# Optimization experiments

Hardware: AMD Instinct MI355X
Metric: run time of the kernel (lower is better)

## Reference

```python
import jax, jax.numpy as jnp
import numpy as np

B, S, D, H = 2, 2048, 512, 8
E = D // H  # per-head depth = 64


def setup_inputs() -> dict:
    key = jax.random.key(0)
    ks = jax.random.split(key, 10)
    x = jax.random.normal(ks[0], (B, S, D), dtype=jnp.float32)
    # binary mask: 1 = masked position (added as -1e9)
    attention_mask = jax.random.randint(ks[1], (B, S, S), 0, 2, dtype=jnp.int32)
    # per-head Dense weights stacked: [H, D, E] (Keras Dense: y = x @ W + b)
    sc = 1.0 / np.sqrt(D)
    Wq = jax.random.normal(ks[2], (H, D, E), dtype=jnp.float32) * sc
    Wk = jax.random.normal(ks[3], (H, D, E), dtype=jnp.float32) * sc
    Wv = jax.random.normal(ks[4], (H, D, E), dtype=jnp.float32) * sc
    bq = jnp.zeros((H, E), dtype=jnp.float32)
    bk = jnp.zeros((H, E), dtype=jnp.float32)
    bv = jnp.zeros((H, E), dtype=jnp.float32)
    Wo = jax.random.normal(ks[5], (D, D), dtype=jnp.float32) * sc
    bo = jnp.zeros((D,), dtype=jnp.float32)
    return {"x": x, "attention_mask": attention_mask, "Wq": Wq, "bq": bq,
            "Wk": Wk, "bk": bk, "Wv": Wv, "bv": bv, "Wo": Wo, "bo": bo}


def reference(x, attention_mask, Wq, bq, Wk, bk, Wv, bv, Wo, bo):
    # Per-head Dense projections, vectorized over heads: [B,H,S,E]
    q = jnp.einsum('bsd,hde->bhse', x, Wq) + bq[None, :, None, :]
    k = jnp.einsum('bsd,hde->bhse', x, Wk) + bk[None, :, None, :]
    v = jnp.einsum('bsd,hde->bhse', x, Wv) + bv[None, :, None, :]
    # scaled dot-product attention
    scores = jnp.einsum('bhse,bhte->bhst', q, k) / jnp.sqrt(jnp.float32(E))
    scores = scores + (-1e9) * attention_mask.astype(jnp.float32)[:, None, :, :]
    weights = jax.nn.softmax(scores, axis=-1)
    o = jnp.einsum('bhst,bhte->bhse', weights, v)
    # concat heads (head i -> columns [i*E:(i+1)*E]) then output Dense
    o = o.transpose(0, 2, 1, 3).reshape(B, S, D)
    return o @ Wo + bo
```

## Files before the change

### kernel.cpp

```cpp
#include <hip/hip_runtime.h>
#include <hip/hip_bf16.h>

typedef unsigned short u16;
typedef unsigned int u32;
typedef unsigned long long u64;
typedef short s16x8 __attribute__((ext_vector_type(8)));
typedef float f32x4 __attribute__((ext_vector_type(4)));
typedef float f32x16 __attribute__((ext_vector_type(16)));
typedef int i32x4 __attribute__((ext_vector_type(4)));

static __device__ __forceinline__ u16 f2b(float f) {
    union { float f; unsigned u; } x; x.f = f;
    unsigned r = x.u + 0x7fffu + ((x.u >> 16) & 1u);
    return (u16)(r >> 16);
}

static __device__ __forceinline__ u32 pkbf2(float a, float b) {
    union { __hip_bfloat162 h; u32 u; } c;
    c.h = __float22bfloat162_rn(make_float2(a, b));
    return c.u;
}

static __device__ __forceinline__ f32x16 zero16() {
    f32x16 z;
#pragma unroll
    for (int i = 0; i < 16; i++) z[i] = 0.f;
    return z;
}

static __device__ __forceinline__ s16x8 mk8(u32 a, u32 b, u32 c, u32 d) {
    union { u32 u[4]; s16x8 v; } x;
    x.u[0] = a; x.u[1] = b; x.u[2] = c; x.u[3] = d;
    return x.v;
}

static __device__ __forceinline__ u32 sx32(u32 v) {
    return (u32)__shfl_xor((int)v, 32, 64);
}

static __device__ __forceinline__ void gll16(const u16* g, u16* l) {
    __builtin_amdgcn_global_load_lds(
        (const __attribute__((address_space(1))) u32*)g,
        (__attribute__((address_space(3))) u32*)l, 16, 0, 0);
}


__global__ __launch_bounds__(256)
void k_pack_all(const float* __restrict__ x,
                const float* __restrict__ Wq, const float* __restrict__ Wk,
                const float* __restrict__ Wv, const float* __restrict__ Wo,
                const float* __restrict__ bq, const float* __restrict__ bk,
                const float* __restrict__ bv, const float* __restrict__ bo,
                u16* __restrict__ xb, u16* __restrict__ WT, u16* __restrict__ WoT,
                float* __restrict__ bias) {
    int idx = blockIdx.x * 256 + threadIdx.x;
    if (idx < 524288) {
        int i = idx * 4;
        float4 v = *(const float4*)(x + i);
        ushort4 o;
        o.x = f2b(v.x); o.y = f2b(v.y); o.z = f2b(v.z); o.w = f2b(v.w);
        *(ushort4*)(xb + i) = o;
    } else if (idx < 1310720) {
        int t = idx - 524288;
        int z = t >> 18, r = t & 262143;
        const float* W = (z == 0) ? Wq : (z == 1) ? Wk : Wv;
        int n = r >> 9, d = r & 511;
        WT[t] = f2b(W[((n >> 6) * 512 + d) * 64 + (n & 63)]);
    } else if (idx < 1572864) {
        int r = idx - 1310720;
        int n = r >> 9, d = r & 511;
        WoT[r] = f2b(Wo[d * 512 + n]);
    } else if (idx < 1574912) {
        int i = idx - 1572864;
        float v;
        if (i < 512) v = bq[i];
        else if (i < 1024) v = bk[i - 512];
        else if (i < 1536) v = bv[i - 1024];
        else v = bo[i - 1536];
        bias[i] = v;
    }
}


template<int MF, bool F32OUT>
__global__ __launch_bounds__(256)
void k_gemm(const u16* __restrict__ A, const u16* __restrict__ BTbase,
            const float* __restrict__ biasBase,
            u16* __restrict__ Cb, u16* __restrict__ Vt, float* __restrict__ Cf,
            const int* __restrict__ mask, u32* __restrict__ mb) {
    const int BM = MF * 32;
    const int nblk = blockIdx.x, mblk = blockIdx.y, z = blockIdx.z;
    const int tid = threadIdx.x;

    if (!F32OUT && z == 3) {
        const int bi = mblk * 4 + nblk;
#pragma unroll
        for (int it = 0; it < 4; it++) {
            const int i2 = bi * 1024 + it * 256 + tid;
            const int* p = mask + (size_t)i2 * 32;
            unsigned wv2 = 0;
#pragma unroll
            for (int j = 0; j < 32; j += 4) {
                int4 v = *(const int4*)(p + j);
                wv2 |= ((unsigned)(v.x & 1) << j) | ((unsigned)(v.y & 1) << (j + 1)) |
                       ((unsigned)(v.z & 1) << (j + 2)) | ((unsigned)(v.w & 1) << (j + 3));
            }
            mb[i2] = wv2;
        }
        return;
    }

    const u16* BT = BTbase + (size_t)z * 262144;
    const float* bias = biasBase + z * 512;
    __shared__ __align__(16) u16 As[MF * 32 * 64];
    __shared__ __align__(16) u16 Bs[128 * 64];
    const int lane = tid & 63, wv = tid >> 6;
    const int lr = lane & 15, lg = lane >> 4;
    const int wr = (wv >> 1) * (MF * 16), wc = (wv & 1) * 64;
    const int lr8 = lane >> 3, lc8 = (lane & 7) ^ lr8;
    const u16* Ag = A + (size_t)(mblk * BM + wv * 8 + lr8) * 512 + lc8 * 8;
    const u16* Bg = BT + (size_t)(nblk * 128 + wv * 8 + lr8) * 512 + lc8 * 8;

    f32x4 acc[MF][4];
#pragma unroll
    for (int i = 0; i < MF; i++)
#pragma unroll
        for (int j = 0; j < 4; j++) acc[i][j] = (f32x4){0.f, 0.f, 0.f, 0.f};

    for (int kt = 0; kt < 8; kt++) {
        __syncthreads();
#pragma unroll
        for (int i = 0; i < MF; i++)
            gll16(Ag + (size_t)(i * 32) * 512 + kt * 64, &As[(i * 32 + wv * 8) * 64]);
#pragma unroll
        for (int i = 0; i < 4; i++)
            gll16(Bg + (size_t)(i * 32) * 512 + kt * 64, &Bs[(i * 32 + wv * 8) * 64]);
        __syncthreads();
#pragma unroll
        for (int ks = 0; ks < 2; ks++) {
            s16x8 af[MF], bf[4];
#pragma unroll
            for (int mf = 0; mf < MF; mf++) {
                int r = wr + mf * 16 + lr;
                af[mf] = *(const s16x8*)&As[r * 64 + ((ks * 32 + lg * 8) ^ ((r & 7) << 3))];
            }
#pragma unroll
            for (int nf = 0; nf < 4; nf++) {
                int r = wc + nf * 16 + lr;
                bf[nf] = *(const s16x8*)&Bs[r * 64 + ((ks * 32 + lg * 8) ^ ((r & 7) << 3))];
            }
#pragma unroll
            for (int mf = 0; mf < MF; mf++)
#pragma unroll
                for (int nf = 0; nf < 4; nf++)
                    acc[mf][nf] = __builtin_amdgcn_mfma_f32_16x16x32_bf16(
                        af[mf], bf[nf], acc[mf][nf], 0, 0, 0);
        }
    }
    const float qsc = (!F32OUT && z == 0) ? 0.18033688011112042f : 1.0f;
#pragma unroll
    for (int nf = 0; nf < 4; nf++) {
        int col = nblk * 128 + wc + nf * 16 + lr;
        float bval = bias[col];
#pragma unroll
        for (int mf = 0; mf < MF; mf++) {
            int row0 = mblk * BM + wr + mf * 16 + lg * 4;
            if (F32OUT) {
#pragma unroll
                for (int r = 0; r < 4; r++)
                    Cf[(size_t)(row0 + r) * 512 + col] = acc[mf][nf][r] + bval;
            } else if (z == 2) {
                ushort4 o;
                o.x = f2b(acc[mf][nf][0] + bval);
                o.y = f2b(acc[mf][nf][1] + bval);
                o.z = f2b(acc[mf][nf][2] + bval);
                o.w = f2b(acc[mf][nf][3] + bval);
                *(ushort4*)(Vt + (size_t)(row0 >> 11) * 1048576 +
                            (size_t)col * 2048 + (row0 & 2047)) = o;
            } else {
#pragma unroll
                for (int r = 0; r < 4; r++)
                    Cb[(size_t)z * 2097152 + (size_t)(row0 + r) * 512 + col] =
                        f2b((acc[mf][nf][r] + bval) * qsc);
            }
        }
    }
}


__global__ __launch_bounds__(256, 2)
void k_attn(const u16* __restrict__ qkv, const u16* __restrict__ vt,
            const u32* __restrict__ mb, u16* __restrict__ oc) {
    const int qt = blockIdx.x, h = blockIdx.y, b = blockIdx.z;
    const u16* Qb = qkv + (size_t)b * 1048576 + h * 64;
    const u16* Kb = Qb + 2097152;
    const u16* VtH = vt + (size_t)b * 1048576 + (size_t)h * 131072;

    __shared__ __align__(16) u16 SMEM[24576];
    __shared__ float Lbuf[4][64];

    const int tid = threadIdx.x;
    const int lane = tid & 63, w = tid >> 6;
    const int hi = lane >> 5, l31 = lane & 31;
    const int qrow = qt * 64 + l31;

    const u32* mbl = mb + (size_t)(b * 2048 + qrow) * 64 + w * 16;
    const u32* mbh = mbl + 2048;
    u32 ML[16], MH[16];
#pragma unroll
    for (int i = 0; i < 4; i++) {
        uint4 a = *(const uint4*)(mbl + 4 * i);
        uint4 c = *(const uint4*)(mbh + 4 * i);
        ML[4 * i] = a.x; ML[4 * i + 1] = a.y; ML[4 * i + 2] = a.z; ML[4 * i + 3] = a.w;
        MH[4 * i] = c.x; MH[4 * i + 1] = c.y; MH[4 * i + 2] = c.z; MH[4 * i + 3] = c.w;
    }

    s16x8 qfl[4], qfh[4];
#pragma unroll
    for (int ks = 0; ks < 4; ks++) {
        qfl[ks] = *(const s16x8*)(Qb + (size_t)qrow * 512 + ks * 16 + hi * 8);
        qfh[ks] = *(const s16x8*)(Qb + (size_t)(qrow + 32) * 512 + ks * 16 + hi * 8);
    }

    const int lr8 = lane >> 3, lc8 = (lane & 7) ^ lr8;
    const int vr16 = lane >> 2, vc4 = (lane & 3) ^ ((lane >> 3) & 3);
    const int kv0 = w * 512;

    const u16* kptr = Kb + (size_t)(kv0 + lr8) * 512 + lc8 * 8;
    const u16* vptr = VtH + (size_t)vr16 * 2048 + kv0 + vc4 * 8;

    u16* wbase = &SMEM[w * 6144];
    u16* Vq = wbase + 4096;

    const int kswz = (l31 & 7) << 3;
    const int vkey = (l31 >> 1) & 3;

#pragma unroll
    for (int i = 0; i < 4; i++)
        gll16(kptr + (size_t)(i * 8) * 512, wbase + i * 512);
#pragma unroll
    for (int i = 0; i < 4; i++)
        gll16(vptr + (size_t)(i * 16) * 2048, Vq + i * 512);
#pragma unroll
    for (int i = 0; i < 4; i++)
        gll16(kptr + (size_t)(32 + i * 8) * 512, wbase + 2048 + i * 512);
    asm volatile("s_waitcnt vmcnt(8)" ::: "memory");
    __builtin_amdgcn_sched_barrier(0);

    f32x16 aL0 = zero16(), aL1 = zero16(), aH0 = zero16(), aH1 = zero16();
    f32x4 lvl = (f32x4){0.f, 0.f, 0.f, 0.f}, lvh = (f32x4){0.f, 0.f, 0.f, 0.f};

    f32x16 sl = zero16(), sh = zero16();
    __builtin_amdgcn_s_setprio(1);
#pragma unroll
    for (int ks = 0; ks < 4; ks++) {
        s16x8 kf = *(const s16x8*)&wbase[l31 * 64 + ((ks * 16 + hi * 8) ^ kswz)];
        sl = __builtin_amdgcn_mfma_f32_32x32x16_bf16(kf, qfl[ks], sl, 0, 0, 0);
        sh = __builtin_amdgcn_mfma_f32_32x32x16_bf16(kf, qfh[ks], sh, 0, 0, 0);
    }
    __builtin_amdgcn_s_setprio(0);

#pragma unroll
    for (int t = 0; t < 16; t++) {
        if (t < 14) {
            const u16* kp = kptr + (size_t)((t + 2) * 32) * 512;
            u16* db = wbase + ((t & 1) << 11);
#pragma unroll
            for (int i = 0; i < 4; i++)
                gll16(kp + (size_t)(i * 8) * 512, db + i * 512);
            asm volatile("s_waitcnt vmcnt(8)" ::: "memory");
        } else if (t == 14) {
            asm volatile("s_waitcnt vmcnt(4)" ::: "memory");
        } else {
            asm volatile("s_waitcnt vmcnt(0)" ::: "memory");
        }
        __builtin_amdgcn_sched_barrier(0);

        f32x16 nl, nh;
        if (t < 15) {
            const u16* Kn = wbase + (((t + 1) & 1) << 11);
            nl = zero16(); nh = zero16();
#pragma unroll
            for (int ks = 0; ks < 4; ks++) {
                s16x8 kf = *(const s16x8*)&Kn[l31 * 64 + ((ks * 16 + hi * 8) ^ kswz)];
                nl = __builtin_amdgcn_mfma_f32_32x32x16_bf16(kf, qfl[ks], nl, 0, 0, 0);
                nh = __builtin_amdgcn_mfma_f32_32x32x16_bf16(kf, qfh[ks], nh, 0, 0, 0);
            }
        }

        s16x8 pal0, pal1, pah0, pah1;
        {
            const u32 mw = ML[t] >> (hi * 4);
            u32 pk[8];
#pragma unroll
            for (int g = 0; g < 8; g++) {
                const int p0 = ((2 * g) & 3) + 8 * (g >> 1);
                float a = ((mw >> p0) & 1u) ? 0.f : __builtin_amdgcn_exp2f(sl[2 * g]);
                float b2 = ((mw >> (p0 + 1)) & 1u) ? 0.f : __builtin_amdgcn_exp2f(sl[2 * g + 1]);
                lvl[(2 * g) & 3] += a;
                lvl[(2 * g + 1) & 3] += b2;
                pk[g] = pkbf2(a, b2);
            }
            u32 xa = sx32(hi ? pk[0] : pk[2]);
            u32 xb = sx32(hi ? pk[1] : pk[3]);
            u32 xc = sx32(hi ? pk[4] : pk[6]);
            u32 xd = sx32(hi ? pk[5] : pk[7]);
            pal0 = hi ? mk8(xa, xb, pk[2], pk[3]) : mk8(pk[0], pk[1], xa, xb);
            pal1 = hi ? mk8(xc, xd, pk[6], pk[7]) : mk8(pk[4], pk[5], xc, xd);
        }
        {
            const u32 mw = MH[t] >> (hi * 4);
            u32 pk[8];
#pragma unroll
            for (int g = 0; g < 8; g++) {
                const int p0 = ((2 * g) & 3) + 8 * (g >> 1);
                float a = ((mw >> p0) & 1u) ? 0.f : __builtin_amdgcn_exp2f(sh[2 * g]);
                float b2 = ((mw >> (p0 + 1)) & 1u) ? 0.f : __builtin_amdgcn_exp2f(sh[2 * g + 1]);
                lvh[(2 * g) & 3] += a;
                lvh[(2 * g + 1) & 3] += b2;
                pk[g] = pkbf2(a, b2);
            }
            u32 xa = sx32(hi ? pk[0] : pk[2]);
            u32 xb = sx32(hi ? pk[1] : pk[3]);
            u32 xc = sx32(hi ? pk[4] : pk[6]);
            u32 xd = sx32(hi ? pk[5] : pk[7]);
            pah0 = hi ? mk8(xa, xb, pk[2], pk[3]) : mk8(pk[0], pk[1], xa, xb);
            pah1 = hi ? mk8(xc, xd, pk[6], pk[7]) : mk8(pk[4], pk[5], xc, xd);
        }

        if (t < 14) asm volatile("s_waitcnt vmcnt(4)" ::: "memory");
        else        asm volatile("s_waitcnt vmcnt(0)" ::: "memory");
        __builtin_amdgcn_sched_barrier(0);

        __builtin_amdgcn_s_setprio(1);
#pragma unroll
        for (int ksg = 0; ksg < 2; ksg++) {
            const int off = ((ksg * 2 + hi) ^ vkey) << 3;
            s16x8 bv0 = *(const s16x8*)&Vq[l31 * 32 + off];
            s16x8 bv1 = *(const s16x8*)&Vq[(32 + l31) * 32 + off];
            s16x8 pl = ksg ? pal1 : pal0;
            s16x8 ph = ksg ? pah1 : pah0;
            aL0 = __builtin_amdgcn_mfma_f32_32x32x16_bf16(pl, bv0, aL0, 0, 0, 0);
            aL1 = __builtin_amdgcn_mfma_f32_32x32x16_bf16(pl, bv1, aL1, 0, 0, 0);
            aH0 = __builtin_amdgcn_mfma_f32_32x32x16_bf16(ph, bv0, aH0, 0, 0, 0);
            aH1 = __builtin_amdgcn_mfma_f32_32x32x16_bf16(ph, bv1, aH1, 0, 0, 0);
        }
        __builtin_amdgcn_s_setprio(0);
        __builtin_amdgcn_sched_barrier(0);

        if (t < 15) {
            const u16* vp = vptr + (t + 1) * 32;
#pragma unroll
            for (int i = 0; i < 4; i++)
                gll16(vp + (size_t)(i * 16) * 2048, Vq + i * 512);
            sl = nl; sh = nh;
        }
    }

    float Lsl = (lvl[0] + lvl[1]) + (lvl[2] + lvl[3]);
    Lsl += __shfl_xor(Lsl, 32, 64);
    float Lsh = (lvh[0] + lvh[1]) + (lvh[2] + lvh[3]);
    Lsh += __shfl_xor(Lsh, 32, 64);
    if (lane < 32) { Lbuf[w][l31] = Lsl; Lbuf[w][32 + l31] = Lsh; }

    float* Obuf = (float*)SMEM;
    const int lx = (lane & 7) * 4;
    const int ob = w * 2048 + lane * 32;
    const int eh = w & 1, gg = w >> 1;
    __syncthreads();

#pragma unroll
    for (int g = 0; g < 4; g++) {
        *(f32x4*)&Obuf[ob + ((4 * g) ^ lx)] =
            (f32x4){aL0[4 * g], aL0[4 * g + 1], aL0[4 * g + 2], aL0[4 * g + 3]};
        *(f32x4*)&Obuf[ob + ((16 + 4 * g) ^ lx)] =
            (f32x4){aL1[4 * g], aL1[4 * g + 1], aL1[4 * g + 2], aL1[4 * g + 3]};
    }
    __syncthreads();
#pragma unroll
    for (int gi = 0; gi < 2; gi++) {
        const int g = gg * 2 + gi;
        const int off = (16 * eh + 4 * g) ^ lx;
        f32x4 s0 = *(const f32x4*)&Obuf[lane * 32 + off];
        f32x4 s1 = *(const f32x4*)&Obuf[2048 + lane * 32 + off];
        f32x4 s2 = *(const f32x4*)&Obuf[4096 + lane * 32 + off];
        f32x4 s3 = *(const f32x4*)&Obuf[6144 + lane * 32 + off];
        f32x4 sum = (s0 + s1) + (s2 + s3);
#pragma unroll
        for (int j = 0; j < 4; j++) {
            const int q = j + 4 * hi + 8 * g;
            float D = Lbuf[0][q] + Lbuf[1][q] + Lbuf[2][q] + Lbuf[3][q];
            const size_t orow = ((size_t)b * 2048 + qt * 64 + q) * 512 + h * 64 + eh * 32;
            oc[orow + l31] = f2b(sum[j] / D);
        }
    }
    __syncthreads();

#pragma unroll
    for (int g = 0; g < 4; g++) {
        *(f32x4*)&Obuf[ob + ((4 * g) ^ lx)] =
            (f32x4){aH0[4 * g], aH0[4 * g + 1], aH0[4 * g + 2], aH0[4 * g + 3]};
        *(f32x4*)&Obuf[ob + ((16 + 4 * g) ^ lx)] =
            (f32x4){aH1[4 * g], aH1[4 * g + 1], aH1[4 * g + 2], aH1[4 * g + 3]};
    }
    __syncthreads();
#pragma unroll
    for (int gi = 0; gi < 2; gi++) {
        const int g = gg * 2 + gi;
        const int off = (16 * eh + 4 * g) ^ lx;
        f32x4 s0 = *(const f32x4*)&Obuf[lane * 32 + off];
        f32x4 s1 = *(const f32x4*)&Obuf[2048 + lane * 32 + off];
        f32x4 s2 = *(const f32x4*)&Obuf[4096 + lane * 32 + off];
        f32x4 s3 = *(const f32x4*)&Obuf[6144 + lane * 32 + off];
        f32x4 sum = (s0 + s1) + (s2 + s3);
#pragma unroll
        for (int j = 0; j < 4; j++) {
            const int q = j + 4 * hi + 8 * g;
            float D = Lbuf[0][32 + q] + Lbuf[1][32 + q] + Lbuf[2][32 + q] + Lbuf[3][32 + q];
            const size_t orow = ((size_t)b * 2048 + qt * 64 + 32 + q) * 512 + h * 64 + eh * 32;
            oc[orow + l31] = f2b(sum[j] / D);
        }
    }
}


extern "C" void kernel_launch(void* const* d_in, const int* in_sizes, int n_in,
                              void* d_out, int out_size, void* d_ws, size_t ws_size,
                              hipStream_t stream) {
    const float* x    = (const float*)d_in[0];
    const int*   mask = (const int*)d_in[1];
    const float* Wq   = (const float*)d_in[2];
    const float* bq   = (const float*)d_in[3];
    const float* Wk   = (const float*)d_in[4];
    const float* bk   = (const float*)d_in[5];
    const float* Wv   = (const float*)d_in[6];
    const float* bv   = (const float*)d_in[7];
    const float* Wo   = (const float*)d_in[8];
    const float* bo   = (const float*)d_in[9];

    u16* xb     = (u16*)d_ws;
    u16* WT     = xb + 2097152;
    u16* WoT    = WT + 786432;
    u16* qkv    = WoT + 262144;
    u16* vtp    = qkv + 4194304;
    u16* oc     = qkv + 6291456;
    float* bias = (float*)(oc + 2097152);
    u32* mbits  = (u32*)(bias + 2048);

    k_pack_all<<<6152, 256, 0, stream>>>(x, Wq, Wk, Wv, Wo, bq, bk, bv, bo,
                                         xb, WT, WoT, bias);
    k_gemm<2, false><<<dim3(4, 64, 4), 256, 0, stream>>>(
        xb, WT, bias, qkv, vtp, nullptr, mask, mbits);
    k_attn<<<dim3(32, 8, 2), 256, 0, stream>>>(qkv, vtp, mbits, oc);
    k_gemm<1, true><<<dim3(4, 128, 1), 256, 0, stream>>>(
        oc, WoT, bias + 1536, nullptr, nullptr, (float*)d_out, nullptr, nullptr);
}
```

Baseline: 70.59 us.

## Double-buffer LDS tiles in projection GEMM with async global-to-LDS prefetch

Turns the single-buffered A/B shared-memory tiles in the projection GEMM into two buffers. The next-but-one K tile is loaded while MFMAs run on the current one. Explicit vmcnt waits and raw s_barrier calls replace the two __syncthreads per iteration, so global-load latency overlaps with compute. The hardcoded vmcnt(6) assumes exactly six outstanding loads per stage (MF+4), and the larger LDS footprint may reduce occupancy.

```diff
diff --git a/kernel.cpp b/kernel.cpp
--- a/kernel.cpp
+++ b/kernel.cpp
@@ -112,8 +112,8 @@
 
     const u16* BT = BTbase + (size_t)z * 262144;
     const float* bias = biasBase + z * 512;
-    __shared__ __align__(16) u16 As[MF * 32 * 64];
-    __shared__ __align__(16) u16 Bs[128 * 64];
+    __shared__ __align__(16) u16 As[2][MF * 32 * 64];
+    __shared__ __align__(16) u16 Bs[2][128 * 64];
     const int lane = tid & 63, wv = tid >> 6;
     const int lr = lane & 15, lg = lane >> 4;
     const int wr = (wv >> 1) * (MF * 16), wc = (wv & 1) * 64;
@@ -127,27 +127,36 @@
 #pragma unroll
         for (int j = 0; j < 4; j++) acc[i][j] = (f32x4){0.f, 0.f, 0.f, 0.f};
 
+#pragma unroll
+    for (int i = 0; i < MF; i++)
+        gll16(Ag + (size_t)(i * 32) * 512, &As[0][(i * 32 + wv * 8) * 64]);
+#pragma unroll
+    for (int i = 0; i < 4; i++)
+        gll16(Bg + (size_t)(i * 32) * 512, &Bs[0][(i * 32 + wv * 8) * 64]);
+#pragma unroll
+    for (int i = 0; i < MF; i++)
+        gll16(Ag + (size_t)(i * 32) * 512 + 64, &As[1][(i * 32 + wv * 8) * 64]);
+#pragma unroll
+    for (int i = 0; i < 4; i++)
+        gll16(Bg + (size_t)(i * 32) * 512 + 64, &Bs[1][(i * 32 + wv * 8) * 64]);
+    asm volatile("s_waitcnt vmcnt(6)" ::: "memory");
+    __builtin_amdgcn_s_barrier();
+    __builtin_amdgcn_sched_barrier(0);
+
     for (int kt = 0; kt < 8; kt++) {
-        __syncthreads();
-#pragma unroll
-        for (int i = 0; i < MF; i++)
-            gll16(Ag + (size_t)(i * 32) * 512 + kt * 64, &As[(i * 32 + wv * 8) * 64]);
-#pragma unroll
-        for (int i = 0; i < 4; i++)
-            gll16(Bg + (size_t)(i * 32) * 512 + kt * 64, &Bs[(i * 32 + wv * 8) * 64]);
-        __syncthreads();
+        const int bo = kt & 1;
 #pragma unroll
         for (int ks = 0; ks < 2; ks++) {
             s16x8 af[MF], bf[4];
 #pragma unroll
             for (int mf = 0; mf < MF; mf++) {
                 int r = wr + mf * 16 + lr;
-                af[mf] = *(const s16x8*)&As[r * 64 + ((ks * 32 + lg * 8) ^ ((r & 7) << 3))];
+                af[mf] = *(const s16x8*)&As[bo][r * 64 + ((ks * 32 + lg * 8) ^ ((r & 7) << 3))];
             }
 #pragma unroll
             for (int nf = 0; nf < 4; nf++) {
                 int r = wc + nf * 16 + lr;
-                bf[nf] = *(const s16x8*)&Bs[r * 64 + ((ks * 32 + lg * 8) ^ ((r & 7) << 3))];
+                bf[nf] = *(const s16x8*)&Bs[bo][r * 64 + ((ks * 32 + lg * 8) ^ ((r & 7) << 3))];
             }
 #pragma unroll
             for (int mf = 0; mf < MF; mf++)
@@ -155,6 +164,25 @@
                 for (int nf = 0; nf < 4; nf++)
                     acc[mf][nf] = __builtin_amdgcn_mfma_f32_16x16x32_bf16(
                         af[mf], bf[nf], acc[mf][nf], 0, 0, 0);
+        }
+        asm volatile("s_waitcnt lgkmcnt(0)" ::: "memory");
+        __builtin_amdgcn_sched_barrier(0);
+        __builtin_amdgcn_s_barrier();
+        __builtin_amdgcn_sched_barrier(0);
+        if (kt < 6) {
+            const int koff = (kt + 2) * 64;
+#pragma unroll
+            for (int i = 0; i < MF; i++)
+                gll16(Ag + (size_t)(i * 32) * 512 + koff, &As[bo][(i * 32 + wv * 8) * 64]);
+#pragma unroll
+            for (int i = 0; i < 4; i++)
+                gll16(Bg + (size_t)(i * 32) * 512 + koff, &Bs[bo][(i * 32 + wv * 8) * 64]);
+        }
+        if (kt < 7) {
+            if (kt < 6) asm volatile("s_waitcnt vmcnt(6)" ::: "memory");
+            else        asm volatile("s_waitcnt vmcnt(0)" ::: "memory");
+            __builtin_amdgcn_s_barrier();
+            __builtin_amdgcn_sched_barrier(0);
         }
     }
     const float qsc = (!F32OUT && z == 0) ? 0.18033688011112042f : 1.0f;
```

New measurement: 71.74 us. About the same (+1.6%).
